# Performance work log

Hardware: AMD Instinct MI355X
Metric: run time of the kernel (lower is better)

Reference implementation:

```python
import jax, jax.numpy as jnp
import numpy as np

N_NODES = 50000
N_EDGES = 600000
N_GRAPHS = 64
IN_DIM = 6
HID = 128


def setup_inputs() -> dict:
    key = jax.random.key(0)
    ks = jax.random.split(key, 10)
    x = jax.random.normal(ks[0], (N_NODES, IN_DIM), dtype=jnp.float32)
    edge_index = jax.random.randint(ks[1], (2, N_EDGES), 0, N_NODES, dtype=jnp.int64)
    batch = jnp.sort(jax.random.randint(ks[2], (N_NODES,), 0, N_GRAPHS, dtype=jnp.int64))
    def glorot(k, shape):
        lim = float(np.sqrt(6.0 / (shape[0] + shape[1])))
        return jax.random.uniform(k, shape, jnp.float32, -lim, lim)
    return {
        'x': x, 'edge_index': edge_index, 'batch': batch,
        'W1': glorot(ks[3], (IN_DIM, HID)), 'b1': jnp.zeros((HID,), jnp.float32),
        'W2': glorot(ks[4], (HID, HID)), 'b2': jnp.zeros((HID,), jnp.float32),
        'W3': glorot(ks[5], (HID, HID)), 'b3': jnp.zeros((HID,), jnp.float32),
        'fc1_w': glorot(ks[6], (HID, 64)), 'fc1_b': jnp.zeros((64,), jnp.float32),
        'fc2_w': glorot(ks[7], (64, 1)), 'fc2_b': jnp.zeros((1,), jnp.float32),
    }


def _gcn_norm(edge_index, n):
    # PyG GCNConv default: add self-loops, symmetric D^-1/2 A D^-1/2 normalization.
    loop = jnp.arange(n, dtype=edge_index.dtype)
    src = jnp.concatenate([edge_index[0], loop])
    dst = jnp.concatenate([edge_index[1], loop])
    deg = jax.ops.segment_sum(jnp.ones_like(dst, dtype=jnp.float32), dst, num_segments=n)
    dis = jnp.where(deg > 0, jax.lax.rsqrt(jnp.maximum(deg, 1.0)), 0.0)
    norm = dis[src] * dis[dst]  # [E+N]
    return src, dst, norm


def _gcn_layer(x, W, b, src, dst, norm, n):
    h = x @ W                       # [N, H] small GEMM
    msg = h[src] * norm[:, None]    # [E+N, H] irregular gather
    out = jax.ops.segment_sum(msg, dst, num_segments=n)  # scatter-add
    return out + b


def reference(x, edge_index, batch, W1, b1, W2, b2, W3, b3, fc1_w, fc1_b, fc2_w, fc2_b):
    n = x.shape[0]
    src, dst, norm = _gcn_norm(edge_index, n)
    h = jax.nn.relu(_gcn_layer(x, W1, b1, src, dst, norm, n))
    h = jax.nn.relu(_gcn_layer(h, W2, b2, src, dst, norm, n))
    h = jax.nn.relu(_gcn_layer(h, W3, b3, src, dst, norm, n))
    # global mean pool over graphs
    sums = jax.ops.segment_sum(h, batch, num_segments=N_GRAPHS)  # [B, H]
    cnt = jax.ops.segment_sum(jnp.ones((n,), jnp.float32), batch, num_segments=N_GRAPHS)
    pooled = sums / jnp.maximum(cnt, 1.0)[:, None]
    z = jax.nn.relu(pooled @ fc1_w + fc1_b)
    return z @ fc2_w + fc2_b  # [B, 1]
```

## Files before the change

### kernel.cpp

```cpp
#include <hip/hip_runtime.h>
#include <hip/hip_fp16.h>

#define HID 128
#define NGRAPH 64
#define CAP 64

typedef unsigned int uint32;
typedef unsigned short ushort;
using short8 = __attribute__((ext_vector_type(8))) short;
using f32x4  = __attribute__((ext_vector_type(4))) float;

__device__ __forceinline__ float2 h2f2(uint32 u) {
    __half2 h = *(__half2*)&u;
    return __half22float2(h);
}
__device__ __forceinline__ uint32 f2h2(float a, float b) {
    __half2 h;
    h.x = __float2half(a);
    h.y = __float2half(b);
    return *(uint32*)&h;
}

__device__ __forceinline__ void accum4(float* acc, uint4 v) {
    float2 e0 = h2f2(v.x), e1 = h2f2(v.y), e2 = h2f2(v.z), e3 = h2f2(v.w);
    acc[0] += e0.x; acc[1] += e0.y; acc[2] += e1.x; acc[3] += e1.y;
    acc[4] += e2.x; acc[5] += e2.y; acc[6] += e3.x; acc[7] += e3.y;
}

__global__ void setup(int* __restrict__ fill, uint32* __restrict__ s1,
                      uint32* __restrict__ s2, int n) {
    int i = blockIdx.x * blockDim.x + threadIdx.x;
    if (i < n) fill[i] = 0;
    if (i < 64) {
        s1[(size_t)n * 64 + i] = 0u;
        s2[(size_t)n * 64 + i] = 0u;
    }
}

__global__ void csr_fill_pack(const int* __restrict__ src, const int* __restrict__ dst,
                              int* __restrict__ fill, int* __restrict__ csr,
                              int E, int EB,
                              const float* __restrict__ W2, const float* __restrict__ W3,
                              ushort* __restrict__ wt) {
    int b = blockIdx.x;
    if (b < EB) {
        int e = b * blockDim.x + threadIdx.x;
        if (e >= E) return;
        int d = dst[e];
        int pos = atomicAdd(&fill[d], 1);
        if (pos < CAP) csr[(size_t)d * CAP + pos] = src[e];
    } else {
        int t = (b - EB) * blockDim.x + threadIdx.x;
        int sel = t >> 14;
        int idx = t & 16383;
        int nn = idx >> 7, kk = idx & 127;
        const float* W = sel ? W3 : W2;
        wt[sel * 16384 + idx] = __half_as_ushort(__float2half(W[kk * HID + nn]));
    }
}

__global__ void finalize(const int* __restrict__ fill, float* __restrict__ dis,
                         const float* __restrict__ x, float4* __restrict__ xp4, int n) {
    int i = blockIdx.x * blockDim.x + threadIdx.x;
    if (i >= n) return;
    int d = fill[i] + 1;
    float di = (float)(1.0 / sqrt((double)d));
    dis[i] = di;
    const float* xi = x + (size_t)i * 6;
    xp4[(size_t)i * 2]     = make_float4(di * xi[0], di * xi[1], di * xi[2], di * xi[3]);
    xp4[(size_t)i * 2 + 1] = make_float4(di * xi[4], di * xi[5], 0.f, 0.f);
}

__global__ __launch_bounds__(256) void layer1_fused(
    const float4* __restrict__ xp4, const int* __restrict__ fill,
    const int* __restrict__ csr, const float* __restrict__ dis,
    const float* __restrict__ W1, const float* __restrict__ b1,
    uint32* __restrict__ S1, int n) {
    int t = blockIdx.x * blockDim.x + threadIdx.x;
    int i = t >> 6, lane = t & 63;
    if (i >= n) return;
    int m = fill[i]; if (m > CAP) m = CAP;
    float a0 = 0.f, a1 = 0.f, a2 = 0.f, a3 = 0.f, a4 = 0.f, a5 = 0.f;
    if (lane < m) {
        int s = csr[(size_t)i * CAP + lane];
        float4 p0 = xp4[(size_t)s * 2];
        float4 p1 = xp4[(size_t)s * 2 + 1];
        a0 = p0.x; a1 = p0.y; a2 = p0.z;
        a3 = p0.w; a4 = p1.x; a5 = p1.y;
    }
#pragma unroll
    for (int off = 32; off > 0; off >>= 1) {
        a0 += __shfl_xor(a0, off); a1 += __shfl_xor(a1, off);
        a2 += __shfl_xor(a2, off); a3 += __shfl_xor(a3, off);
        a4 += __shfl_xor(a4, off); a5 += __shfl_xor(a5, off);
    }
    float di = dis[i];
    float4 s0 = xp4[(size_t)i * 2];
    float4 s1 = xp4[(size_t)i * 2 + 1];
    float xa[6];
    xa[0] = di * (s0.x + a0); xa[1] = di * (s0.y + a1);
    xa[2] = di * (s0.z + a2); xa[3] = di * (s0.w + a3);
    xa[4] = di * (s1.x + a4); xa[5] = di * (s1.y + a5);
    int c0 = lane * 2;
    float z0 = b1[c0], z1 = b1[c0 + 1];
#pragma unroll
    for (int k = 0; k < 6; ++k) {
        z0 += xa[k] * W1[k * HID + c0];
        z1 += xa[k] * W1[k * HID + c0 + 1];
    }
    S1[(size_t)i * 64 + lane] = f2h2(di * fmaxf(z0, 0.f), di * fmaxf(z1, 0.f));
}

__global__ __launch_bounds__(256, 5) void layer_agg_gemm(
    const uint32* __restrict__ Sin, const int* __restrict__ fill,
    const int* __restrict__ csr, const float* __restrict__ dis,
    const ushort* __restrict__ WT, const float* __restrict__ bias,
    uint32* __restrict__ Sout, int n, int scaleOut) {
    __shared__ uint4 plds4[32 * 17];
    const int wave = threadIdx.x >> 6;
    const int lane = threadIdx.x & 63;
    const int grp = lane >> 4;
    const int q   = lane & 15;
    const int blk0 = blockIdx.x * 32;
    const int base = blk0 + wave * 8;

    int mt8[8];
    int idx8[8];
#pragma unroll
    for (int j = 0; j < 8; ++j) {
        int i = base + j;
        int fv = (i < n) ? fill[i] : 0;
        int m = fv > CAP ? CAP : fv;
        idx8[j] = (lane < m) ? csr[(size_t)i * CAP + lane]
                             : ((lane == m && i < n && m < CAP) ? i : n);
        mt8[j] = m + (m < CAP ? 1 : 0);
    }

#pragma unroll
    for (int jp = 0; jp < 4; ++jp) {
        const int ja = jp * 2, jb = ja + 1;
        float acca[8] = {0.f, 0.f, 0.f, 0.f, 0.f, 0.f, 0.f, 0.f};
        float accb[8] = {0.f, 0.f, 0.f, 0.f, 0.f, 0.f, 0.f, 0.f};
        {
            int sa1 = __shfl(idx8[ja], grp);
            int sa2 = __shfl(idx8[ja], 4 + grp);
            int sa3 = __shfl(idx8[ja], 8 + grp);
            int sa4 = __shfl(idx8[ja], 12 + grp);
            int sb1 = __shfl(idx8[jb], grp);
            int sb2 = __shfl(idx8[jb], 4 + grp);
            int sb3 = __shfl(idx8[jb], 8 + grp);
            int sb4 = __shfl(idx8[jb], 12 + grp);
            uint4 va1 = *(const uint4*)(Sin + (size_t)sa1 * 64 + q * 4);
            uint4 va2 = *(const uint4*)(Sin + (size_t)sa2 * 64 + q * 4);
            uint4 va3 = *(const uint4*)(Sin + (size_t)sa3 * 64 + q * 4);
            uint4 va4 = *(const uint4*)(Sin + (size_t)sa4 * 64 + q * 4);
            uint4 vb1 = *(const uint4*)(Sin + (size_t)sb1 * 64 + q * 4);
            uint4 vb2 = *(const uint4*)(Sin + (size_t)sb2 * 64 + q * 4);
            uint4 vb3 = *(const uint4*)(Sin + (size_t)sb3 * 64 + q * 4);
            uint4 vb4 = *(const uint4*)(Sin + (size_t)sb4 * 64 + q * 4);
            accum4(acca, va1); accum4(acca, va2);
            accum4(acca, va3); accum4(acca, va4);
            accum4(accb, vb1); accum4(accb, vb2);
            accum4(accb, vb3); accum4(accb, vb4);
        }
        for (int k = 16; k < mt8[ja]; k += 16) {
            int s1 = __shfl(idx8[ja], k + grp);
            int s2 = __shfl(idx8[ja], k + 4 + grp);
            int s3 = __shfl(idx8[ja], k + 8 + grp);
            int s4 = __shfl(idx8[ja], k + 12 + grp);
            uint4 v1 = *(const uint4*)(Sin + (size_t)s1 * 64 + q * 4);
            uint4 v2 = *(const uint4*)(Sin + (size_t)s2 * 64 + q * 4);
            uint4 v3 = *(const uint4*)(Sin + (size_t)s3 * 64 + q * 4);
            uint4 v4 = *(const uint4*)(Sin + (size_t)s4 * 64 + q * 4);
            accum4(acca, v1); accum4(acca, v2);
            accum4(acca, v3); accum4(acca, v4);
        }
        for (int k = 16; k < mt8[jb]; k += 16) {
            int s1 = __shfl(idx8[jb], k + grp);
            int s2 = __shfl(idx8[jb], k + 4 + grp);
            int s3 = __shfl(idx8[jb], k + 8 + grp);
            int s4 = __shfl(idx8[jb], k + 12 + grp);
            uint4 v1 = *(const uint4*)(Sin + (size_t)s1 * 64 + q * 4);
            uint4 v2 = *(const uint4*)(Sin + (size_t)s2 * 64 + q * 4);
            uint4 v3 = *(const uint4*)(Sin + (size_t)s3 * 64 + q * 4);
            uint4 v4 = *(const uint4*)(Sin + (size_t)s4 * 64 + q * 4);
            accum4(accb, v1); accum4(accb, v2);
            accum4(accb, v3); accum4(accb, v4);
        }
#pragma unroll
        for (int r = 0; r < 8; ++r) {
            acca[r] += __shfl_xor(acca[r], 16);
            acca[r] += __shfl_xor(acca[r], 32);
            accb[r] += __shfl_xor(accb[r], 16);
            accb[r] += __shfl_xor(accb[r], 32);
        }
        if (grp == 0) {
            int ia = base + ja, ib = base + jb;
            float da = (ia < n) ? dis[ia] : 0.f;
            float db = (ib < n) ? dis[ib] : 0.f;
            plds4[(wave * 8 + ja) * 17 + q] =
                make_uint4(f2h2(da * acca[0], da * acca[1]),
                           f2h2(da * acca[2], da * acca[3]),
                           f2h2(da * acca[4], da * acca[5]),
                           f2h2(da * acca[6], da * acca[7]));
            plds4[(wave * 8 + jb) * 17 + q] =
                make_uint4(f2h2(db * accb[0], db * accb[1]),
                           f2h2(db * accb[2], db * accb[3]),
                           f2h2(db * accb[4], db * accb[5]),
                           f2h2(db * accb[6], db * accb[7]));
        }
    }
    __syncthreads();

    const int l16 = lane & 15, quad = lane >> 4;
    f32x4 acc2[2][2] = {};
#pragma unroll
    for (int kc = 0; kc < 4; ++kc) {
        int ko = kc * 32 + quad * 8;
        short8 a0 = *(const short8*)&plds4[(size_t)l16 * 17 + kc * 4 + quad];
        short8 a1 = *(const short8*)&plds4[(size_t)(16 + l16) * 17 + kc * 4 + quad];
#pragma unroll
        for (int ct = 0; ct < 2; ++ct) {
            short8 wh = *(const short8*)(WT + (size_t)(wave * 32 + ct * 16 + l16) * HID + ko);
            acc2[0][ct] = __builtin_amdgcn_mfma_f32_16x16x32_f16(wh, a0, acc2[0][ct], 0, 0, 0);
            acc2[1][ct] = __builtin_amdgcn_mfma_f32_16x16x32_f16(wh, a1, acc2[1][ct], 0, 0, 0);
        }
    }
    ushort* so = (ushort*)Sout;
#pragma unroll
    for (int rt = 0; rt < 2; ++rt) {
        int node = blk0 + rt * 16 + l16;
        if (node >= n) continue;
        float sc = scaleOut ? dis[node] : 1.f;
#pragma unroll
        for (int ct = 0; ct < 2; ++ct) {
            int cb = wave * 32 + ct * 16 + quad * 4;
            float4 bv = *(const float4*)(bias + cb);
            float o0 = fmaxf(acc2[rt][ct][0] + bv.x, 0.f) * sc;
            float o1 = fmaxf(acc2[rt][ct][1] + bv.y, 0.f) * sc;
            float o2 = fmaxf(acc2[rt][ct][2] + bv.z, 0.f) * sc;
            float o3 = fmaxf(acc2[rt][ct][3] + bv.w, 0.f) * sc;
            *(uint2*)(so + (size_t)node * HID + cb) = make_uint2(f2h2(o0, o1), f2h2(o2, o3));
        }
    }
}

__global__ __launch_bounds__(256) void pool_head(
    const uint32* __restrict__ h, const int* __restrict__ batch,
    const float* __restrict__ fc1w, const float* __restrict__ fc1b,
    const float* __restrict__ fc2w, const float* __restrict__ fc2b,
    float* __restrict__ out, int n) {
    __shared__ float red[4][128];
    __shared__ float pp[128];
    const int g = blockIdx.x;
    const int t = threadIdx.x;
    const int sub = t >> 6, c = t & 63;

    int lo0 = 0, hi0 = n, lo1 = 0, hi1 = n;
    while (lo0 < hi0 || lo1 < hi1) {
        if (lo0 < hi0) {
            int mid = (lo0 + hi0) >> 1;
            if (batch[mid] < g) lo0 = mid + 1; else hi0 = mid;
        }
        if (lo1 < hi1) {
            int mid = (lo1 + hi1) >> 1;
            if (batch[mid] < g + 1) lo1 = mid + 1; else hi1 = mid;
        }
    }
    const int start = lo0, end = lo1;

    float sx = 0.f, sy = 0.f;
    int i = start + sub;
    for (; i + 12 < end; i += 16) {
        uint32 u0 = h[(size_t)i * 64 + c];
        uint32 u1 = h[(size_t)(i + 4) * 64 + c];
        uint32 u2 = h[(size_t)(i + 8) * 64 + c];
        uint32 u3 = h[(size_t)(i + 12) * 64 + c];
        float2 v0 = h2f2(u0), v1 = h2f2(u1), v2 = h2f2(u2), v3 = h2f2(u3);
        sx += v0.x + v1.x + v2.x + v3.x;
        sy += v0.y + v1.y + v2.y + v3.y;
    }
    for (; i < end; i += 4) {
        float2 v = h2f2(h[(size_t)i * 64 + c]);
        sx += v.x; sy += v.y;
    }
    *(float2*)&red[sub][2 * c] = make_float2(sx, sy);
    __syncthreads();

    if (t < 64) {
        float2 r0 = *(float2*)&red[0][2 * t];
        float2 r1 = *(float2*)&red[1][2 * t];
        float2 r2 = *(float2*)&red[2][2 * t];
        float2 r3 = *(float2*)&red[3][2 * t];
        float inv = 1.0f / fmaxf((float)(end - start), 1.0f);
        pp[2 * t]     = (r0.x + r1.x + r2.x + r3.x) * inv;
        pp[2 * t + 1] = (r0.y + r1.y + r2.y + r3.y) * inv;
        float z = fc1b[t];
#pragma unroll 8
        for (int k = 0; k < HID; ++k) z += pp[k] * fc1w[k * 64 + t];
        z = fmaxf(z, 0.f);
        float v = z * fc2w[t];
#pragma unroll
        for (int off = 32; off > 0; off >>= 1) v += __shfl_down(v, off);
        if (t == 0) out[g] = v + fc2b[0];
    }
}

extern "C" void kernel_launch(void* const* d_in, const int* in_sizes, int n_in,
                              void* d_out, int out_size, void* d_ws, size_t ws_size,
                              hipStream_t stream) {
    const float* x     = (const float*)d_in[0];
    const int*   ei    = (const int*)d_in[1];
    const int*   batch = (const int*)d_in[2];
    const float* W1    = (const float*)d_in[3];
    const float* b1    = (const float*)d_in[4];
    const float* W2    = (const float*)d_in[5];
    const float* b2    = (const float*)d_in[6];
    const float* W3    = (const float*)d_in[7];
    const float* b3    = (const float*)d_in[8];
    const float* fc1w  = (const float*)d_in[9];
    const float* fc1b  = (const float*)d_in[10];
    const float* fc2w  = (const float*)d_in[11];
    const float* fc2b  = (const float*)d_in[12];
    float* out = (float*)d_out;

    const int N = in_sizes[0] / 6;
    const int E = in_sizes[1] / 2;
    const int* src = ei;
    const int* dst = ei + E;

    char* ws = (char*)d_ws;
    char* p = ws;
    uint32* S1   = (uint32*)p;   p += (size_t)(N + 1) * 256;
    uint32* S2   = (uint32*)p;   p += (size_t)(N + 1) * 256;
    uint32* B1h  = (uint32*)p;   p += (size_t)N * 256;
    float4* xp4  = (float4*)p;   p += (size_t)N * 32;
    ushort* WT   = (ushort*)p;   p += 2 * 32768;
    float* dis     = (float*)p;  p += (size_t)N * 4;
    int*   fill    = (int*)p;    p += (size_t)N * 4;
    int*   csr     = (int*)p;    p += (size_t)N * CAP * 4;

    const int B = 256;
    const int EB = (E + B - 1) / B;

    setup<<<(N + B - 1) / B, B, 0, stream>>>(fill, S1, S2, N);
    csr_fill_pack<<<EB + 128, B, 0, stream>>>(src, dst, fill, csr, E, EB, W2, W3, WT);
    finalize<<<(N + B - 1) / B, B, 0, stream>>>(fill, dis, x, xp4, N);

    int nodeWaveBlocks = (int)(((size_t)N * 64 + B - 1) / B);
    int fusedBlocks = (N + 31) / 32;

    layer1_fused<<<nodeWaveBlocks, B, 0, stream>>>(xp4, fill, csr, dis, W1, b1, S1, N);

    layer_agg_gemm<<<fusedBlocks, B, 0, stream>>>(S1, fill, csr, dis, WT, b2, S2, N, 1);

    layer_agg_gemm<<<fusedBlocks, B, 0, stream>>>(S2, fill, csr, dis, WT + 16384, b3, B1h, N, 0);

    pool_head<<<NGRAPH, B, 0, stream>>>(B1h, batch, fc1w, fc1b, fc2w, fc2b, out, N);
}
```

Baseline: 236.5 us.

## Make per-wave GEMM independent of block barrier; precompute graph boundaries in setup

The aggregation+GEMM kernel now has each wave do its own 8-node MFMA GEMM over all 128 output columns using a private LDS slice padded with zero rows, so the block-wide __syncthreads is removed. Waves no longer wait on the slowest gather in the block, but each wave now wastes half of each 16-row MFMA tile and loads the full weight matrix (4x more WT reads per wave). Separately, graph start offsets are computed once in the setup kernel, replacing the per-block binary search in pool_head.

Measured after the change: 270.3 us. 1.14x slower.

```diff
diff --git a/kernel.cpp b/kernel.cpp
--- a/kernel.cpp
+++ b/kernel.cpp
@@ -28,12 +28,25 @@
 }
 
 __global__ void setup(int* __restrict__ fill, uint32* __restrict__ s1,
-                      uint32* __restrict__ s2, int n) {
+                      uint32* __restrict__ s2, const int* __restrict__ batch,
+                      int* __restrict__ gstart, int n) {
     int i = blockIdx.x * blockDim.x + threadIdx.x;
     if (i < n) fill[i] = 0;
     if (i < 64) {
         s1[(size_t)n * 64 + i] = 0u;
         s2[(size_t)n * 64 + i] = 0u;
+    }
+    if (i < n) {
+        int b0 = batch[i];
+        if (i == 0) {
+            for (int g = 0; g <= b0; ++g) gstart[g] = 0;
+        }
+        if (i + 1 < n) {
+            int b1 = batch[i + 1];
+            for (int g = b0 + 1; g <= b1; ++g) gstart[g] = i + 1;
+        } else {
+            for (int g = b0 + 1; g <= NGRAPH; ++g) gstart[g] = n;
+        }
     }
 }
 
@@ -116,13 +129,16 @@
     const int* __restrict__ csr, const float* __restrict__ dis,
     const ushort* __restrict__ WT, const float* __restrict__ bias,
     uint32* __restrict__ Sout, int n, int scaleOut) {
-    __shared__ uint4 plds4[32 * 17];
+    __shared__ uint4 plds4[4][16 * 17];
     const int wave = threadIdx.x >> 6;
     const int lane = threadIdx.x & 63;
     const int grp = lane >> 4;
     const int q   = lane & 15;
-    const int blk0 = blockIdx.x * 32;
-    const int base = blk0 + wave * 8;
+    const int base = blockIdx.x * 32 + wave * 8;
+
+    uint4 z4 = make_uint4(0u, 0u, 0u, 0u);
+    plds4[wave][(8 + grp) * 17 + q] = z4;
+    plds4[wave][(12 + grp) * 17 + q] = z4;
 
     int mt8[8];
     int idx8[8];
@@ -198,55 +214,49 @@
             int ia = base + ja, ib = base + jb;
             float da = (ia < n) ? dis[ia] : 0.f;
             float db = (ib < n) ? dis[ib] : 0.f;
-            plds4[(wave * 8 + ja) * 17 + q] =
+            plds4[wave][ja * 17 + q] =
                 make_uint4(f2h2(da * acca[0], da * acca[1]),
                            f2h2(da * acca[2], da * acca[3]),
                            f2h2(da * acca[4], da * acca[5]),
                            f2h2(da * acca[6], da * acca[7]));
-            plds4[(wave * 8 + jb) * 17 + q] =
+            plds4[wave][jb * 17 + q] =
                 make_uint4(f2h2(db * accb[0], db * accb[1]),
                            f2h2(db * accb[2], db * accb[3]),
                            f2h2(db * accb[4], db * accb[5]),
                            f2h2(db * accb[6], db * accb[7]));
         }
     }
-    __syncthreads();
 
     const int l16 = lane & 15, quad = lane >> 4;
-    f32x4 acc2[2][2] = {};
-#pragma unroll
-    for (int kc = 0; kc < 4; ++kc) {
-        int ko = kc * 32 + quad * 8;
-        short8 a0 = *(const short8*)&plds4[(size_t)l16 * 17 + kc * 4 + quad];
-        short8 a1 = *(const short8*)&plds4[(size_t)(16 + l16) * 17 + kc * 4 + quad];
-#pragma unroll
-        for (int ct = 0; ct < 2; ++ct) {
-            short8 wh = *(const short8*)(WT + (size_t)(wave * 32 + ct * 16 + l16) * HID + ko);
-            acc2[0][ct] = __builtin_amdgcn_mfma_f32_16x16x32_f16(wh, a0, acc2[0][ct], 0, 0, 0);
-            acc2[1][ct] = __builtin_amdgcn_mfma_f32_16x16x32_f16(wh, a1, acc2[1][ct], 0, 0, 0);
-        }
-    }
+    const int node = base + l16;
+    const bool live = (l16 < 8) && (node < n);
+    float sc = 1.f;
+    if (live && scaleOut) sc = dis[node];
     ushort* so = (ushort*)Sout;
 #pragma unroll
-    for (int rt = 0; rt < 2; ++rt) {
-        int node = blk0 + rt * 16 + l16;
-        if (node >= n) continue;
-        float sc = scaleOut ? dis[node] : 1.f;
-#pragma unroll
-        for (int ct = 0; ct < 2; ++ct) {
-            int cb = wave * 32 + ct * 16 + quad * 4;
+    for (int ct = 0; ct < 8; ++ct) {
+        f32x4 acc = {};
+#pragma unroll
+        for (int kc = 0; kc < 4; ++kc) {
+            int ko = kc * 32 + quad * 8;
+            short8 a0 = *(const short8*)&plds4[wave][(size_t)l16 * 17 + kc * 4 + quad];
+            short8 wh = *(const short8*)(WT + (size_t)(ct * 16 + l16) * HID + ko);
+            acc = __builtin_amdgcn_mfma_f32_16x16x32_f16(wh, a0, acc, 0, 0, 0);
+        }
+        if (live) {
+            int cb = ct * 16 + quad * 4;
             float4 bv = *(const float4*)(bias + cb);
-            float o0 = fmaxf(acc2[rt][ct][0] + bv.x, 0.f) * sc;
-            float o1 = fmaxf(acc2[rt][ct][1] + bv.y, 0.f) * sc;
-            float o2 = fmaxf(acc2[rt][ct][2] + bv.z, 0.f) * sc;
-            float o3 = fmaxf(acc2[rt][ct][3] + bv.w, 0.f) * sc;
+            float o0 = fmaxf(acc[0] + bv.x, 0.f) * sc;
+            float o1 = fmaxf(acc[1] + bv.y, 0.f) * sc;
+            float o2 = fmaxf(acc[2] + bv.z, 0.f) * sc;
+            float o3 = fmaxf(acc[3] + bv.w, 0.f) * sc;
             *(uint2*)(so + (size_t)node * HID + cb) = make_uint2(f2h2(o0, o1), f2h2(o2, o3));
         }
     }
 }
 
 __global__ __launch_bounds__(256) void pool_head(
-    const uint32* __restrict__ h, const int* __restrict__ batch,
+    const uint32* __restrict__ h, const int* __restrict__ gstart,
     const float* __restrict__ fc1w, const float* __restrict__ fc1b,
     const float* __restrict__ fc2w, const float* __restrict__ fc2b,
     float* __restrict__ out, int n) {
@@ -256,18 +266,7 @@
     const int t = threadIdx.x;
     const int sub = t >> 6, c = t & 63;
 
-    int lo0 = 0, hi0 = n, lo1 = 0, hi1 = n;
-    while (lo0 < hi0 || lo1 < hi1) {
-        if (lo0 < hi0) {
-            int mid = (lo0 + hi0) >> 1;
-            if (batch[mid] < g) lo0 = mid + 1; else hi0 = mid;
-        }
-        if (lo1 < hi1) {
-            int mid = (lo1 + hi1) >> 1;
-            if (batch[mid] < g + 1) lo1 = mid + 1; else hi1 = mid;
-        }
-    }
-    const int start = lo0, end = lo1;
+    const int start = gstart[g], end = gstart[g + 1];
 
     float sx = 0.f, sy = 0.f;
     int i = start + sub;
@@ -339,11 +338,12 @@
     float* dis     = (float*)p;  p += (size_t)N * 4;
     int*   fill    = (int*)p;    p += (size_t)N * 4;
     int*   csr     = (int*)p;    p += (size_t)N * CAP * 4;
+    int*   gstart  = (int*)p;    p += (NGRAPH + 1) * 4;
 
     const int B = 256;
     const int EB = (E + B - 1) / B;
 
-    setup<<<(N + B - 1) / B, B, 0, stream>>>(fill, S1, S2, N);
+    setup<<<(N + B - 1) / B, B, 0, stream>>>(fill, S1, S2, batch, gstart, N);
     csr_fill_pack<<<EB + 128, B, 0, stream>>>(src, dst, fill, csr, E, EB, W2, W3, WT);
     finalize<<<(N + B - 1) / B, B, 0, stream>>>(fill, dis, x, xp4, N);
 
@@ -356,5 +356,5 @@
 
     layer_agg_gemm<<<fusedBlocks, B, 0, stream>>>(S2, fill, csr, dis, WT + 16384, b3, B1h, N, 0);
 
-    pool_head<<<NGRAPH, B, 0, stream>>>(B1h, batch, fc1w, fc1b, fc2w, fc2b, out, N);
-}
+    pool_head<<<NGRAPH, B, 0, stream>>>(B1h, gstart, fc1w, fc1b, fc2w, fc2b, out, N);
+}
```
